# Kernel tuning notes

Hardware: AMD Instinct MI355X
Metric: run time of the kernel (lower is better)

## Reference

```python
import jax, jax.numpy as jnp
import numpy as np

D_MODEL = 4096
EXPERTS = 64
TOPK = 2


def setup_inputs() -> dict:
    key = jax.random.key(0)
    kx, kw = jax.random.split(key)
    x = jax.random.normal(kx, (4, 4096, D_MODEL), dtype=jnp.float32)
    # nn.Linear(input_size, expert_num, bias=False) weight, stored as [D, E] for x @ W
    W = jax.random.normal(kw, (D_MODEL, EXPERTS), dtype=jnp.float32) * (1.0 / np.sqrt(D_MODEL))
    return {"x": x, "W": W}


def reference(x, W):
    # logits = GateL(x): [B, S, E]
    logits = jnp.einsum("bsd,de->bse", x, W)
    y = jax.nn.softmax(logits, axis=-1)
    # top-k mask: scatter ones at top-k expert slots, zero elsewhere
    _, topk_idx = jax.lax.top_k(y, TOPK)            # [B, S, k]
    mask = jnp.sum(jax.nn.one_hot(topk_idx, EXPERTS, dtype=y.dtype), axis=-2)  # [B, S, E]
    y = y * mask
    return (y, logits)
```

## Files before the change

### kernel.cpp

```cpp
#include <hip/hip_runtime.h>
#include <hip/hip_bf16.h>


typedef float f32x4 __attribute__((ext_vector_type(4)));
typedef __bf16 bf16x8 __attribute__((ext_vector_type(8)));

#define MFMA16(a, b, c) __builtin_amdgcn_mfma_f32_16x16x32_bf16((a), (b), (c), 0, 0, 0)

__global__ __launch_bounds__(256) void k_prep_w(const float* __restrict__ W,
                                                __bf16* __restrict__ wsW) {
  const int kc = blockIdx.x;
  const int t = threadIdx.x;
  const int kk0 = t >> 4;
  const int n0 = (t & 15) << 2;
  for (int i = 0; i < 2; ++i) {
    const int kk = kk0 + (i << 4);
    const float4 w4 = *(const float4*)(W + (size_t)(kc * 32 + kk) * 64 + n0);
    const float f[4] = {w4.x, w4.y, w4.z, w4.w};
    for (int j = 0; j < 4; ++j) {
      const int n = n0 + j;
      const __bf16 h = (__bf16)f[j];
      const __bf16 l = (__bf16)(f[j] - (float)h);
      const int base = (kc << 12) + ((n >> 4) << 9) + ((n & 15) << 5) + kk;
      wsW[base] = h;
      wsW[base + 2048] = l;
    }
  }
}

__device__ __forceinline__ void cvt_store(char* xb, int m, int lk, float4 v) {
  const int off = ((m >> 4) << 10) | ((m & 15) << 6) | ((lk >> 3) << 4) | ((lk & 7) << 1);
  const float f0 = v.x, f1 = v.y, f2 = v.z, f3 = v.w;
  const __bf16 h0 = (__bf16)f0, h1 = (__bf16)f1, h2 = (__bf16)f2, h3 = (__bf16)f3;
  const __bf16 l0 = (__bf16)(f0 - (float)h0), l1 = (__bf16)(f1 - (float)h1);
  const __bf16 l2 = (__bf16)(f2 - (float)h2), l3 = (__bf16)(f3 - (float)h3);
  uint2 uh, ul;
  uh.x = (unsigned)__builtin_bit_cast(unsigned short, h0) |
         ((unsigned)__builtin_bit_cast(unsigned short, h1) << 16);
  uh.y = (unsigned)__builtin_bit_cast(unsigned short, h2) |
         ((unsigned)__builtin_bit_cast(unsigned short, h3) << 16);
  ul.x = (unsigned)__builtin_bit_cast(unsigned short, l0) |
         ((unsigned)__builtin_bit_cast(unsigned short, l1) << 16);
  ul.y = (unsigned)__builtin_bit_cast(unsigned short, l2) |
         ((unsigned)__builtin_bit_cast(unsigned short, l3) << 16);
  *(uint2*)(xb + off) = uh;
  *(uint2*)(xb + 4096 + off) = ul;
}

__global__ __launch_bounds__(256, 2) void k_gemm(const float* __restrict__ x,
                                                 const __bf16* __restrict__ wsW,
                                                 float* __restrict__ logits) {
  __shared__ __align__(16) char smem[32768];
  char* xs = smem;
  char* wsb = smem + 16384;

  const int t = threadIdx.x;
  const int blk = blockIdx.x;
  const int mb = blk >> 1;
  const int ks = blk & 1;
  const size_t gm0 = (size_t)mb * 64;
  const int kc0 = ks << 6;

  const int lm = t >> 3;
  const int lk = (t & 7) << 2;
  const float* xg = x + (gm0 + lm) * 4096 + (size_t)kc0 * 32 + lk;
  const char* wg = (const char*)wsW + (size_t)kc0 * 8192;
  const int wOffA = t << 4;
  const int wOffB = 4096 + (t << 4);

  const int w = t >> 6, l = t & 63;
  const int mtb = (w & 1) << 1;
  const int ntb = (w >> 1) << 1;
  const int tileoff = ((l & 15) << 6) + ((l >> 4) << 4);

  f32x4 acc00 = {0.f, 0.f, 0.f, 0.f};
  f32x4 acc01 = {0.f, 0.f, 0.f, 0.f};
  f32x4 acc10 = {0.f, 0.f, 0.f, 0.f};
  f32x4 acc11 = {0.f, 0.f, 0.f, 0.f};

  float4 xr0 = *(const float4*)(xg);
  float4 xr1 = *(const float4*)(xg + 32 * 4096);
  uint4 wr0 = *(const uint4*)(wg + wOffA);
  uint4 wr1 = *(const uint4*)(wg + wOffB);

  for (int c = 0; c < 64; ++c) {
    char* xb = xs + ((c & 1) << 13);
    char* wb = wsb + ((c & 1) << 13);
    cvt_store(xb, lm, lk, xr0);
    cvt_store(xb, lm + 32, lk, xr1);
    *(uint4*)(wb + wOffA) = wr0;
    *(uint4*)(wb + wOffB) = wr1;
    __syncthreads();
    if (c < 63) {
      xr0 = *(const float4*)(xg + (c + 1) * 32);
      xr1 = *(const float4*)(xg + (c + 1) * 32 + 32 * 4096);
      wr0 = *(const uint4*)(wg + (c + 1) * 8192 + wOffA);
      wr1 = *(const uint4*)(wg + (c + 1) * 8192 + wOffB);
    }
    const bf16x8 ah0 = *(const bf16x8*)(xb + (mtb + 0) * 1024 + tileoff);
    const bf16x8 ah1 = *(const bf16x8*)(xb + (mtb + 1) * 1024 + tileoff);
    const bf16x8 al0 = *(const bf16x8*)(xb + 4096 + (mtb + 0) * 1024 + tileoff);
    const bf16x8 al1 = *(const bf16x8*)(xb + 4096 + (mtb + 1) * 1024 + tileoff);
    const bf16x8 bh0 = *(const bf16x8*)(wb + (ntb + 0) * 1024 + tileoff);
    const bf16x8 bh1 = *(const bf16x8*)(wb + (ntb + 1) * 1024 + tileoff);
    const bf16x8 bl0 = *(const bf16x8*)(wb + 4096 + (ntb + 0) * 1024 + tileoff);
    const bf16x8 bl1 = *(const bf16x8*)(wb + 4096 + (ntb + 1) * 1024 + tileoff);
    acc00 = MFMA16(ah0, bh0, acc00); acc00 = MFMA16(al0, bh0, acc00);
    acc00 = MFMA16(ah0, bl0, acc00); acc00 = MFMA16(al0, bl0, acc00);
    acc01 = MFMA16(ah0, bh1, acc01); acc01 = MFMA16(al0, bh1, acc01);
    acc01 = MFMA16(ah0, bl1, acc01); acc01 = MFMA16(al0, bl1, acc01);
    acc10 = MFMA16(ah1, bh0, acc10); acc10 = MFMA16(al1, bh0, acc10);
    acc10 = MFMA16(ah1, bl0, acc10); acc10 = MFMA16(al1, bl0, acc10);
    acc11 = MFMA16(ah1, bh1, acc11); acc11 = MFMA16(al1, bh1, acc11);
    acc11 = MFMA16(ah1, bl1, acc11); acc11 = MFMA16(al1, bl1, acc11);
    __syncthreads();
  }

  float* lbase = logits + gm0 * 64;
  const int q = (l >> 4) << 2, ln = l & 15;
  for (int r = 0; r < 4; ++r) {
    const int m0 = (mtb + 0) * 16 + q + r;
    const int m1 = (mtb + 1) * 16 + q + r;
    atomicAdd(lbase + (size_t)m0 * 64 + (ntb + 0) * 16 + ln, acc00[r]);
    atomicAdd(lbase + (size_t)m0 * 64 + (ntb + 1) * 16 + ln, acc01[r]);
    atomicAdd(lbase + (size_t)m1 * 64 + (ntb + 0) * 16 + ln, acc10[r]);
    atomicAdd(lbase + (size_t)m1 * 64 + (ntb + 1) * 16 + ln, acc11[r]);
  }
}

__global__ __launch_bounds__(256) void k_softmax_top2(const float* __restrict__ logits,
                                                      float* __restrict__ y) {
  const int t = threadIdx.x, w = t >> 6, l = t & 63;
  const size_t tok0 = (size_t)blockIdx.x * 64 + w * 16;
  for (int i = 0; i < 16; ++i) {
    const size_t tok = tok0 + i;
    const float v = logits[tok * 64 + l];
    float bv = v; int bi = l;
    for (int off = 32; off > 0; off >>= 1) {
      const float ov = __shfl_xor(bv, off);
      const int oi = __shfl_xor(bi, off);
      if (ov > bv || (ov == bv && oi < bi)) { bv = ov; bi = oi; }
    }
    const int i1 = bi;
    const float m1 = bv;
    float cv = (l == i1) ? -3.402823466e38f : v;
    int ci = l;
    for (int off = 32; off > 0; off >>= 1) {
      const float ov = __shfl_xor(cv, off);
      const int oi = __shfl_xor(ci, off);
      if (ov > cv || (ov == cv && oi < ci)) { cv = ov; ci = oi; }
    }
    const int i2 = ci;
    const float e = __expf(v - m1);
    float s = e;
    for (int off = 32; off > 0; off >>= 1) s += __shfl_xor(s, off);
    y[tok * 64 + l] = ((l == i1) || (l == i2)) ? (e / s) : 0.0f;
  }
}

extern "C" void kernel_launch(void* const* d_in, const int* in_sizes, int n_in,
                              void* d_out, int out_size, void* d_ws, size_t ws_size,
                              hipStream_t stream) {
  (void)in_sizes; (void)n_in; (void)out_size; (void)ws_size;
  const float* x = (const float*)d_in[0];
  const float* W = (const float*)d_in[1];
  float* out = (float*)d_out;
  float* yout = out;
  float* logits = out + 1048576;
  __bf16* wsW = (__bf16*)d_ws;

  k_prep_w<<<128, 256, 0, stream>>>(W, wsW);
  hipMemsetAsync(logits, 0, 4194304, stream);
  k_gemm<<<512, 256, 0, stream>>>(x, wsW, logits);
  k_softmax_top2<<<256, 256, 0, stream>>>(logits, yout);
}
```

Baseline: 412.2 us.

## Fuse gate GEMM with softmax/top-2, load operands directly to registers

Replaces the split-K GEMM, memset, atomics and separate softmax kernel with one fused kernel. Each block computes 32 tokens over the full K, loading x and pre-split W fragments straight from global memory into registers with two-stage software pipelining, so there is no LDS staging and no barriers in the main loop. The low*low MFMA term is dropped (three products instead of four). Logits are stored directly and also staged in LDS so the block can apply softmax and the top-2 mask in place. The trade-offs are fewer blocks (512 blocks of 32 tokens, no K split), uncoalesced per-lane global loads of W, and slightly lower precision from the dropped term.

```diff
diff --git a/kernel.cpp b/kernel.cpp
--- a/kernel.cpp
+++ b/kernel.cpp
@@ -28,115 +28,82 @@
   }
 }
 
-__device__ __forceinline__ void cvt_store(char* xb, int m, int lk, float4 v) {
-  const int off = ((m >> 4) << 10) | ((m & 15) << 6) | ((lk >> 3) << 4) | ((lk & 7) << 1);
-  const float f0 = v.x, f1 = v.y, f2 = v.z, f3 = v.w;
-  const __bf16 h0 = (__bf16)f0, h1 = (__bf16)f1, h2 = (__bf16)f2, h3 = (__bf16)f3;
-  const __bf16 l0 = (__bf16)(f0 - (float)h0), l1 = (__bf16)(f1 - (float)h1);
-  const __bf16 l2 = (__bf16)(f2 - (float)h2), l3 = (__bf16)(f3 - (float)h3);
-  uint2 uh, ul;
-  uh.x = (unsigned)__builtin_bit_cast(unsigned short, h0) |
-         ((unsigned)__builtin_bit_cast(unsigned short, h1) << 16);
-  uh.y = (unsigned)__builtin_bit_cast(unsigned short, h2) |
-         ((unsigned)__builtin_bit_cast(unsigned short, h3) << 16);
-  ul.x = (unsigned)__builtin_bit_cast(unsigned short, l0) |
-         ((unsigned)__builtin_bit_cast(unsigned short, l1) << 16);
-  ul.y = (unsigned)__builtin_bit_cast(unsigned short, l2) |
-         ((unsigned)__builtin_bit_cast(unsigned short, l3) << 16);
-  *(uint2*)(xb + off) = uh;
-  *(uint2*)(xb + 4096 + off) = ul;
-}
+__global__ __launch_bounds__(256, 2) void k_gate(const float* __restrict__ x,
+                                                 const __bf16* __restrict__ wsW,
+                                                 float* __restrict__ y,
+                                                 float* __restrict__ logits) {
+  const int t = threadIdx.x;
+  const int w = t >> 6, l = t & 63;
+  const int tb = blockIdx.x * 32;
+  const int mt = w & 1, nh = w >> 1;
+  const int q = l >> 4, ln = l & 15;
 
-__global__ __launch_bounds__(256, 2) void k_gemm(const float* __restrict__ x,
-                                                 const __bf16* __restrict__ wsW,
-                                                 float* __restrict__ logits) {
-  __shared__ __align__(16) char smem[32768];
-  char* xs = smem;
-  char* wsb = smem + 16384;
+  const float* xp = x + (size_t)(tb + mt * 16 + ln) * 4096 + q * 8;
+  const __bf16* wp = wsW + (nh * 2) * 512 + ln * 32 + q * 8;
 
-  const int t = threadIdx.x;
-  const int blk = blockIdx.x;
-  const int mb = blk >> 1;
-  const int ks = blk & 1;
-  const size_t gm0 = (size_t)mb * 64;
-  const int kc0 = ks << 6;
+  f32x4 acc0 = {0.f, 0.f, 0.f, 0.f};
+  f32x4 acc1 = {0.f, 0.f, 0.f, 0.f};
 
-  const int lm = t >> 3;
-  const int lk = (t & 7) << 2;
-  const float* xg = x + (gm0 + lm) * 4096 + (size_t)kc0 * 32 + lk;
-  const char* wg = (const char*)wsW + (size_t)kc0 * 8192;
-  const int wOffA = t << 4;
-  const int wOffB = 4096 + (t << 4);
+  float4 xa0, xb0, xa1, xb1;
+  bf16x8 h0_0, l0_0, h1_0, l1_0;
+  bf16x8 h0_1, l0_1, h1_1, l1_1;
 
-  const int w = t >> 6, l = t & 63;
-  const int mtb = (w & 1) << 1;
-  const int ntb = (w >> 1) << 1;
-  const int tileoff = ((l & 15) << 6) + ((l >> 4) << 4);
+#define LOAD_STAGE(S, c) do {                                          \
+    xa##S = *(const float4*)(xp + (size_t)(c) * 32);                   \
+    xb##S = *(const float4*)(xp + (size_t)(c) * 32 + 4);               \
+    h0_##S = *(const bf16x8*)(wp + (size_t)(c) * 4096);                \
+    l0_##S = *(const bf16x8*)(wp + (size_t)(c) * 4096 + 2048);         \
+    h1_##S = *(const bf16x8*)(wp + (size_t)(c) * 4096 + 512);          \
+    l1_##S = *(const bf16x8*)(wp + (size_t)(c) * 4096 + 2560);         \
+  } while (0)
 
-  f32x4 acc00 = {0.f, 0.f, 0.f, 0.f};
-  f32x4 acc01 = {0.f, 0.f, 0.f, 0.f};
-  f32x4 acc10 = {0.f, 0.f, 0.f, 0.f};
-  f32x4 acc11 = {0.f, 0.f, 0.f, 0.f};
+#define COMPUTE(S) do {                                                \
+    bf16x8 ah, al;                                                     \
+    const float f[8] = {xa##S.x, xa##S.y, xa##S.z, xa##S.w,            \
+                        xb##S.x, xb##S.y, xb##S.z, xb##S.w};           \
+    _Pragma("unroll")                                                  \
+    for (int i = 0; i < 8; ++i) {                                      \
+      const __bf16 hh = (__bf16)f[i];                                  \
+      ah[i] = hh;                                                      \
+      al[i] = (__bf16)(f[i] - (float)hh);                              \
+    }                                                                  \
+    acc0 = MFMA16(ah, h0_##S, acc0);                                   \
+    acc0 = MFMA16(al, h0_##S, acc0);                                   \
+    acc0 = MFMA16(ah, l0_##S, acc0);                                   \
+    acc1 = MFMA16(ah, h1_##S, acc1);                                   \
+    acc1 = MFMA16(al, h1_##S, acc1);                                   \
+    acc1 = MFMA16(ah, l1_##S, acc1);                                   \
+  } while (0)
 
-  float4 xr0 = *(const float4*)(xg);
-  float4 xr1 = *(const float4*)(xg + 32 * 4096);
-  uint4 wr0 = *(const uint4*)(wg + wOffA);
-  uint4 wr1 = *(const uint4*)(wg + wOffB);
+  LOAD_STAGE(0, 0);
+  LOAD_STAGE(1, 1);
+  for (int c = 0; c < 128; c += 2) {
+    COMPUTE(0);
+    if (c + 2 < 128) LOAD_STAGE(0, c + 2);
+    COMPUTE(1);
+    if (c + 3 < 128) LOAD_STAGE(1, c + 3);
+  }
+#undef LOAD_STAGE
+#undef COMPUTE
 
-  for (int c = 0; c < 64; ++c) {
-    char* xb = xs + ((c & 1) << 13);
-    char* wb = wsb + ((c & 1) << 13);
-    cvt_store(xb, lm, lk, xr0);
-    cvt_store(xb, lm + 32, lk, xr1);
-    *(uint4*)(wb + wOffA) = wr0;
-    *(uint4*)(wb + wOffB) = wr1;
-    __syncthreads();
-    if (c < 63) {
-      xr0 = *(const float4*)(xg + (c + 1) * 32);
-      xr1 = *(const float4*)(xg + (c + 1) * 32 + 32 * 4096);
-      wr0 = *(const uint4*)(wg + (c + 1) * 8192 + wOffA);
-      wr1 = *(const uint4*)(wg + (c + 1) * 8192 + wOffB);
-    }
-    const bf16x8 ah0 = *(const bf16x8*)(xb + (mtb + 0) * 1024 + tileoff);
-    const bf16x8 ah1 = *(const bf16x8*)(xb + (mtb + 1) * 1024 + tileoff);
-    const bf16x8 al0 = *(const bf16x8*)(xb + 4096 + (mtb + 0) * 1024 + tileoff);
-    const bf16x8 al1 = *(const bf16x8*)(xb + 4096 + (mtb + 1) * 1024 + tileoff);
-    const bf16x8 bh0 = *(const bf16x8*)(wb + (ntb + 0) * 1024 + tileoff);
-    const bf16x8 bh1 = *(const bf16x8*)(wb + (ntb + 1) * 1024 + tileoff);
-    const bf16x8 bl0 = *(const bf16x8*)(wb + 4096 + (ntb + 0) * 1024 + tileoff);
-    const bf16x8 bl1 = *(const bf16x8*)(wb + 4096 + (ntb + 1) * 1024 + tileoff);
-    acc00 = MFMA16(ah0, bh0, acc00); acc00 = MFMA16(al0, bh0, acc00);
-    acc00 = MFMA16(ah0, bl0, acc00); acc00 = MFMA16(al0, bl0, acc00);
-    acc01 = MFMA16(ah0, bh1, acc01); acc01 = MFMA16(al0, bh1, acc01);
-    acc01 = MFMA16(ah0, bl1, acc01); acc01 = MFMA16(al0, bl1, acc01);
-    acc10 = MFMA16(ah1, bh0, acc10); acc10 = MFMA16(al1, bh0, acc10);
-    acc10 = MFMA16(ah1, bl0, acc10); acc10 = MFMA16(al1, bl0, acc10);
-    acc11 = MFMA16(ah1, bh1, acc11); acc11 = MFMA16(al1, bh1, acc11);
-    acc11 = MFMA16(ah1, bl1, acc11); acc11 = MFMA16(al1, bl1, acc11);
-    __syncthreads();
+  __shared__ float lt[32 * 65];
+  const int col = nh * 32 + ln;
+#pragma unroll
+  for (int r = 0; r < 4; ++r) {
+    const int row = mt * 16 + q * 4 + r;
+    lt[row * 65 + col] = acc0[r];
+    lt[row * 65 + col + 16] = acc1[r];
+    logits[(size_t)(tb + row) * 64 + col] = acc0[r];
+    logits[(size_t)(tb + row) * 64 + col + 16] = acc1[r];
   }
+  __syncthreads();
 
-  float* lbase = logits + gm0 * 64;
-  const int q = (l >> 4) << 2, ln = l & 15;
-  for (int r = 0; r < 4; ++r) {
-    const int m0 = (mtb + 0) * 16 + q + r;
-    const int m1 = (mtb + 1) * 16 + q + r;
-    atomicAdd(lbase + (size_t)m0 * 64 + (ntb + 0) * 16 + ln, acc00[r]);
-    atomicAdd(lbase + (size_t)m0 * 64 + (ntb + 1) * 16 + ln, acc01[r]);
-    atomicAdd(lbase + (size_t)m1 * 64 + (ntb + 0) * 16 + ln, acc10[r]);
-    atomicAdd(lbase + (size_t)m1 * 64 + (ntb + 1) * 16 + ln, acc11[r]);
-  }
-}
-
-__global__ __launch_bounds__(256) void k_softmax_top2(const float* __restrict__ logits,
-                                                      float* __restrict__ y) {
-  const int t = threadIdx.x, w = t >> 6, l = t & 63;
-  const size_t tok0 = (size_t)blockIdx.x * 64 + w * 16;
-  for (int i = 0; i < 16; ++i) {
-    const size_t tok = tok0 + i;
-    const float v = logits[tok * 64 + l];
+#pragma unroll
+  for (int i = 0; i < 8; ++i) {
+    const int tok = w * 8 + i;
+    const float v = lt[tok * 65 + l];
     float bv = v; int bi = l;
-    for (int off = 32; off > 0; off >>= 1) {
+    for (int off = 32; off; off >>= 1) {
       const float ov = __shfl_xor(bv, off);
       const int oi = __shfl_xor(bi, off);
       if (ov > bv || (ov == bv && oi < bi)) { bv = ov; bi = oi; }
@@ -145,16 +112,15 @@
     const float m1 = bv;
     float cv = (l == i1) ? -3.402823466e38f : v;
     int ci = l;
-    for (int off = 32; off > 0; off >>= 1) {
+    for (int off = 32; off; off >>= 1) {
       const float ov = __shfl_xor(cv, off);
       const int oi = __shfl_xor(ci, off);
       if (ov > cv || (ov == cv && oi < ci)) { cv = ov; ci = oi; }
     }
-    const int i2 = ci;
     const float e = __expf(v - m1);
     float s = e;
-    for (int off = 32; off > 0; off >>= 1) s += __shfl_xor(s, off);
-    y[tok * 64 + l] = ((l == i1) || (l == i2)) ? (e / s) : 0.0f;
+    for (int off = 32; off; off >>= 1) s += __shfl_xor(s, off);
+    y[(size_t)(tb + tok) * 64 + l] = (l == i1 || l == ci) ? (e / s) : 0.0f;
   }
 }
 
@@ -170,7 +136,5 @@
   __bf16* wsW = (__bf16*)d_ws;
 
   k_prep_w<<<128, 256, 0, stream>>>(W, wsW);
-  hipMemsetAsync(logits, 0, 4194304, stream);
-  k_gemm<<<512, 256, 0, stream>>>(x, wsW, logits);
-  k_softmax_top2<<<256, 256, 0, stream>>>(logits, yout);
+  k_gate<<<512, 256, 0, stream>>>(x, wsW, yout, logits);
 }
```

New measurement: 409.9 us. Within noise of the previous version (-0.6%).
